# Kernel optimization log

Measured on AMD Instinct MI355X. Metric: run time of the kernel, lower is better.

## Reference

```python
import jax, jax.numpy as jnp
import numpy as np

C_CURV = 1.0
SQRT_C = C_CURV ** 0.5
MAX_NORM = 1.0 / SQRT_C - 1e-5  # project eps == dist clamp eps == 1e-5
EPS = 1e-15


def setup_inputs() -> dict:
    key = jax.random.key(0)
    k1, k2 = jax.random.split(key)
    B, C, D = 4096, 8192, 256
    # points well inside the unit ball: ||x|| ~ 0.05*sqrt(D) ~ 0.8
    x = jax.random.normal(k1, (B, D), dtype=jnp.float32) * 0.05
    # matches nn.Parameter(torch.randn(C, D) * 0.01)
    proto_tangent = jax.random.normal(k2, (C, D), dtype=jnp.float32) * 0.01
    log_scale = jnp.zeros((C,), dtype=jnp.float32)
    return {"x": x, "proto_tangent": proto_tangent, "log_scale": log_scale}


def _expmap0_project(v):
    # exp_0(v) = tanh(sqrt(c)||v||) v / (sqrt(c)||v||), then project onto ball
    vn = jnp.maximum(jnp.linalg.norm(v, axis=-1, keepdims=True), EPS)
    p = jnp.tanh(SQRT_C * vn) * v / (SQRT_C * vn)
    pn = jnp.linalg.norm(p, axis=-1, keepdims=True)
    return jnp.where(pn > MAX_NORM, p / pn * MAX_NORM, p)


def reference(x, proto_tangent, log_scale):
    protos = _expmap0_project(proto_tangent)          # [C, D]
    c = C_CURV
    # mobius_add(-x, y) broadcast over [B, C]; we only need its norm, so use
    # ||a*(-x) + b*y||^2 = a^2||x||^2 - 2ab<x,y> + b^2||y||^2 (same math,
    # avoids materializing the [B, C, D] intermediate the torch code builds).
    x2 = jnp.sum(x * x, axis=-1)[:, None]             # [B, 1]
    y2 = jnp.sum(protos * protos, axis=-1)[None, :]   # [1, C]
    xy = x @ protos.T                                  # [B, C]  <x, y>
    nxy = -xy                                          # <-x, y>
    a = 1.0 + 2.0 * c * nxy + c * y2                   # coeff of (-x)
    b = 1.0 - c * x2                                   # coeff of y
    denom = jnp.maximum(1.0 + 2.0 * c * nxy + (c * c) * x2 * y2, EPS)
    num_sq = a * a * x2 + 2.0 * a * b * nxy + b * b * y2
    norm = jnp.sqrt(jnp.maximum(num_sq, 0.0)) / denom  # ||mobius_add(-x,y)||
    # project clamp (eps=1e-5) and dist clamp (1/sqrt(c)-1e-5) coincide
    norm = jnp.minimum(norm, MAX_NORM)
    dists = (2.0 / SQRT_C) * jnp.arctanh(SQRT_C * norm)  # [B, C]
    return -dists * jnp.exp(log_scale)[None, :]
```

## Files before the change

### kernel.cpp

```cpp
#include <hip/hip_runtime.h>
#include <hip/hip_bf16.h>
#include <cstdint>

#define MAX_NORM (1.0f - 1e-5f)
#define LN2 0.69314718056f
#define WMAX ((1.0f + MAX_NORM) / (1.0f - MAX_NORM))

typedef __attribute__((ext_vector_type(8))) short bf16x8;
typedef __attribute__((ext_vector_type(4))) float f32x4;

__device__ __forceinline__ unsigned short f2bf(float f) {
  union { float f; unsigned int u; } c; c.f = f;
  unsigned int r = c.u + 0x7fffu + ((c.u >> 16) & 1u);
  return (unsigned short)(r >> 16);
}

__device__ __forceinline__ void gld16(const unsigned short* g, unsigned short* l) {
  __builtin_amdgcn_global_load_lds(
      (const __attribute__((address_space(1))) unsigned int*)g,
      (__attribute__((address_space(3))) unsigned int*)l, 16, 0, 0);
}

__global__ void prep_all(const float* __restrict__ x, const float* __restrict__ pt,
                         const float* __restrict__ ls,
                         unsigned short* __restrict__ xbf, unsigned short* __restrict__ pbf,
                         float* __restrict__ x2, float* __restrict__ fx,
                         float* __restrict__ gy, float* __restrict__ hy,
                         float* __restrict__ es2, int M, int N, int D) {
  int row = blockIdx.x * (blockDim.x >> 6) + (threadIdx.x >> 6);
  int lane = threadIdx.x & 63;
  if (row >= M + N) return;
  const bool isX = row < M;
  const int r = isX ? row : row - M;
  const float* src = (isX ? x : pt) + (size_t)r * D;
  f32x4 v = ((const f32x4*)src)[lane];
  float ss = v[0]*v[0] + v[1]*v[1] + v[2]*v[2] + v[3]*v[3];
  #pragma unroll
  for (int off = 32; off >= 1; off >>= 1) ss += __shfl_xor(ss, off);
  float scale = 1.0f;
  float outsq = ss;
  if (!isX) {
    float vn  = sqrtf(ss);
    float vnc = fmaxf(vn, 1e-15f);
    float th  = tanhf(vnc);
    scale = th / vnc;
    float pn = scale * vn;
    if (pn > MAX_NORM) { float pr = MAX_NORM / pn; scale *= pr; pn = MAX_NORM; }
    outsq = pn * pn;
  }
  unsigned short* dst = (isX ? xbf : pbf) + (size_t)r * D + lane * 4;
  unsigned long long pk =
        (unsigned long long)f2bf(v[0]*scale)
      | ((unsigned long long)f2bf(v[1]*scale) << 16)
      | ((unsigned long long)f2bf(v[2]*scale) << 32)
      | ((unsigned long long)f2bf(v[3]*scale) << 48);
  *(unsigned long long*)dst = pk;
  if (lane == 0) {
    if (isX) {
      x2[r] = outsq;
      fx[r] = 2.0f / (1.0f - outsq);
    } else {
      float g = 1.0f / (1.0f - outsq);
      gy[r]  = g;
      hy[r]  = g * outsq;
      es2[r] = -__expf(ls[r]) * LN2;
    }
  }
}

__global__ __launch_bounds__(256, 2)
void hyp_gemm(const unsigned short* __restrict__ xbf,
              const unsigned short* __restrict__ pbf,
              const float* __restrict__ x2, const float* __restrict__ fx,
              const float* __restrict__ gy, const float* __restrict__ hy,
              const float* __restrict__ es2, float* __restrict__ out,
              int M, int N, int K) {
  __shared__ __align__(16) unsigned short As[2][2][128 * 32];
  __shared__ __align__(16) unsigned short Bs[2][2][128 * 32];
  const int t    = threadIdx.x;
  const int wv   = t >> 6;
  const int lane = t & 63;
  const int wr   = wv >> 1, wc = wv & 1;
  const int frow = lane & 15, kgrp = lane >> 4;
  const int nTM  = M >> 7;
  const int tileM = blockIdx.x % nTM;
  const int tileN = blockIdx.x / nTM;
  const int gr0 = tileM * 128 + wr * 64;
  const int gc0 = tileN * 128 + wc * 64;
  const int NT  = K >> 6;

  f32x4 acc[4][4];
  #pragma unroll
  for (int m = 0; m < 4; ++m)
    #pragma unroll
    for (int n = 0; n < 4; ++n) acc[m][n] = (f32x4){0.f, 0.f, 0.f, 0.f};

  const int srow  = wv * 16 + (lane >> 2);
  const int skoff = (lane & 3) * 8;
  const unsigned short* gA = xbf + (size_t)(tileM * 128 + srow) * K + skoff;
  const unsigned short* gB = pbf + (size_t)(tileN * 128 + srow) * K + skoff;
  const size_t rskip = (size_t)64 * K;

#define STAGE(b, kt)                                                           \
  {                                                                            \
    _Pragma("unroll")                                                          \
    for (int p = 0; p < 2; ++p) {                                              \
      _Pragma("unroll")                                                        \
      for (int j = 0; j < 2; ++j) {                                            \
        gld16(gA + (size_t)j * rskip + (kt) * 64 + p * 32,                     \
              &As[b][p][(j * 64 + wv * 16) * 32]);                             \
        gld16(gB + (size_t)j * rskip + (kt) * 64 + p * 32,                     \
              &Bs[b][p][(j * 64 + wv * 16) * 32]);                             \
      }                                                                        \
    }                                                                          \
  }

#define COMPUTE(b)                                                             \
  {                                                                            \
    _Pragma("unroll")                                                          \
    for (int p = 0; p < 2; ++p) {                                              \
      bf16x8 af[4], bg[4];                                                     \
      _Pragma("unroll")                                                        \
      for (int m = 0; m < 4; ++m)                                              \
        af[m] = *(const bf16x8*)&As[b][p][(wr * 64 + m * 16 + frow) * 32 + kgrp * 8]; \
      _Pragma("unroll")                                                        \
      for (int n = 0; n < 4; ++n)                                              \
        bg[n] = *(const bf16x8*)&Bs[b][p][(wc * 64 + n * 16 + frow) * 32 + kgrp * 8]; \
      _Pragma("unroll")                                                        \
      for (int m = 0; m < 4; ++m)                                              \
        _Pragma("unroll")                                                      \
        for (int n = 0; n < 4; ++n)                                            \
          acc[m][n] = __builtin_amdgcn_mfma_f32_16x16x32_bf16(bg[n], af[m], acc[m][n], 0, 0, 0); \
    }                                                                          \
  }

  STAGE(0, 0);
  __syncthreads();
  int cur = 0;
  for (int kt = 0; kt < NT; ++kt) {
    if (kt + 1 < NT) STAGE(cur ^ 1, kt + 1);
    COMPUTE(cur);
    __syncthreads();
    cur ^= 1;
  }
#undef STAGE
#undef COMPUTE

  float x2s[4], fxs[4];
  #pragma unroll
  for (int m = 0; m < 4; ++m) {
    x2s[m] = x2[gr0 + m * 16 + frow];
    fxs[m] = fx[gr0 + m * 16 + frow];
  }
  #pragma unroll
  for (int n = 0; n < 4; ++n) {
    const int c0 = gc0 + n * 16 + kgrp * 4;
    f32x4 gv = *(const f32x4*)(gy  + c0);
    f32x4 hv = *(const f32x4*)(hy  + c0);
    f32x4 ev = *(const f32x4*)(es2 + c0);
    #pragma unroll
    for (int m = 0; m < 4; ++m) {
      f32x4 a4 = acc[m][n];
      f32x4 o;
      #pragma unroll
      for (int r = 0; r < 4; ++r) {
        float xy = a4[r];
        float u  = fmaf(fxs[m], fmaf(gv[r], fmaf(-2.0f, xy, x2s[m]), hv[r]), 1.0f);
        float t2 = fmaxf(fmaf(u, u, -1.0f), 0.0f);
        float w  = u + __builtin_amdgcn_sqrtf(t2);
        w = fminf(w, WMAX);
        o[r] = ev[r] * __log2f(w);
      }
      *(f32x4*)&out[(size_t)(gr0 + m * 16 + frow) * N + c0] = o;
    }
  }
}

extern "C" void kernel_launch(void* const* d_in, const int* in_sizes, int n_in,
                              void* d_out, int out_size, void* d_ws, size_t ws_size,
                              hipStream_t stream) {
  const float* x  = (const float*)d_in[0];
  const float* pt = (const float*)d_in[1];
  const float* ls = (const float*)d_in[2];
  const int Csz = in_sizes[2];
  const int D   = in_sizes[1] / Csz;
  const int Bsz = in_sizes[0] / D;
  const int M = Bsz, N = Csz, K = D;
  float* outp = (float*)d_out;

  char* ws = (char*)d_ws;
  unsigned short* xbf = (unsigned short*)ws; ws += (size_t)M * K * 2;
  unsigned short* pbf = (unsigned short*)ws; ws += (size_t)N * K * 2;
  float* x2  = (float*)ws; ws += (size_t)M * 4;
  float* fx  = (float*)ws; ws += (size_t)M * 4;
  float* gy  = (float*)ws; ws += (size_t)N * 4;
  float* hy  = (float*)ws; ws += (size_t)N * 4;
  float* es2 = (float*)ws; ws += (size_t)N * 4;

  hipLaunchKernelGGL(prep_all, dim3((M + N + 3) / 4), dim3(256), 0, stream,
                     x, pt, ls, xbf, pbf, x2, fx, gy, hy, es2, M, N, K);
  hipLaunchKernelGGL(hyp_gemm, dim3((M / 128) * (N / 128)), dim3(256), 0, stream,
                     xbf, pbf, x2, fx, gy, hy, es2, outp, M, N, K);
}
```

Baseline: 55.58 us.

## Switch GEMM to 32x32x16 MFMA tiles with XOR-swizzled LDS layout

Replaces the 16x16x32 bf16 MFMA tiling (4x4 accumulators per wave) with 32x32x16 MFMA (2x2 f32x16 accumulators). The LDS fill order for the k-chunks is XOR-swizzled so the 32-row fragment reads avoid bank conflicts. The epilogue is remapped to the 32x32 output layout. The aim is fewer LDS fragment loads and a denser MFMA issue. The risk is a different epilogue store pattern and swizzle mistakes that could break correctness.

```diff
diff --git a/kernel.cpp b/kernel.cpp
--- a/kernel.cpp
+++ b/kernel.cpp
@@ -8,6 +8,7 @@
 
 typedef __attribute__((ext_vector_type(8))) short bf16x8;
 typedef __attribute__((ext_vector_type(4))) float f32x4;
+typedef __attribute__((ext_vector_type(16))) float f32x16;
 
 __device__ __forceinline__ unsigned short f2bf(float f) {
   union { float f; unsigned int u; } c; c.f = f;
@@ -81,7 +82,7 @@
   const int wv   = t >> 6;
   const int lane = t & 63;
   const int wr   = wv >> 1, wc = wv & 1;
-  const int frow = lane & 15, kgrp = lane >> 4;
+  const int l31  = lane & 31, hi = lane >> 5;
   const int nTM  = M >> 7;
   const int tileM = blockIdx.x % nTM;
   const int tileN = blockIdx.x / nTM;
@@ -89,17 +90,19 @@
   const int gc0 = tileN * 128 + wc * 64;
   const int NT  = K >> 6;
 
-  f32x4 acc[4][4];
-  #pragma unroll
-  for (int m = 0; m < 4; ++m)
+  f32x16 acc[2][2];
+  #pragma unroll
+  for (int m = 0; m < 2; ++m)
     #pragma unroll
-    for (int n = 0; n < 4; ++n) acc[m][n] = (f32x4){0.f, 0.f, 0.f, 0.f};
+    for (int n = 0; n < 2; ++n) acc[m][n] = (f32x16)(0.0f);
 
   const int srow  = wv * 16 + (lane >> 2);
-  const int skoff = (lane & 3) * 8;
+  const int skoff = ((lane & 3) ^ (((lane >> 3) & 1) << 1)) * 8;
   const unsigned short* gA = xbf + (size_t)(tileM * 128 + srow) * K + skoff;
   const unsigned short* gB = pbf + (size_t)(tileN * 128 + srow) * K + skoff;
   const size_t rskip = (size_t)64 * K;
+
+  const int rswz = ((lane >> 1) & 1) << 1;
 
 #define STAGE(b, kt)                                                           \
   {                                                                            \
@@ -119,18 +122,23 @@
   {                                                                            \
     _Pragma("unroll")                                                          \
     for (int p = 0; p < 2; ++p) {                                              \
-      bf16x8 af[4], bg[4];                                                     \
+      bf16x8 af[2][2], bg[2][2];                                               \
       _Pragma("unroll")                                                        \
-      for (int m = 0; m < 4; ++m)                                              \
-        af[m] = *(const bf16x8*)&As[b][p][(wr * 64 + m * 16 + frow) * 32 + kgrp * 8]; \
+      for (int m = 0; m < 2; ++m)                                              \
+        _Pragma("unroll")                                                      \
+        for (int ks = 0; ks < 2; ++ks) {                                       \
+          const int kqa = (ks * 2 + hi) ^ rswz;                                \
+          af[m][ks] = *(const bf16x8*)&As[b][p][(wr * 64 + m * 32 + l31) * 32 + kqa * 8]; \
+          bg[m][ks] = *(const bf16x8*)&Bs[b][p][(wc * 64 + m * 32 + l31) * 32 + kqa * 8]; \
+        }                                                                      \
       _Pragma("unroll")                                                        \
-      for (int n = 0; n < 4; ++n)                                              \
-        bg[n] = *(const bf16x8*)&Bs[b][p][(wc * 64 + n * 16 + frow) * 32 + kgrp * 8]; \
-      _Pragma("unroll")                                                        \
-      for (int m = 0; m < 4; ++m)                                              \
+      for (int m = 0; m < 2; ++m)                                              \
         _Pragma("unroll")                                                      \
-        for (int n = 0; n < 4; ++n)                                            \
-          acc[m][n] = __builtin_amdgcn_mfma_f32_16x16x32_bf16(bg[n], af[m], acc[m][n], 0, 0, 0); \
+        for (int n = 0; n < 2; ++n)                                            \
+          _Pragma("unroll")                                                    \
+          for (int ks = 0; ks < 2; ++ks)                                       \
+            acc[m][n] = __builtin_amdgcn_mfma_f32_32x32x16_bf16(               \
+                bg[n][ks], af[m][ks], acc[m][n], 0, 0, 0);                     \
     }                                                                          \
   }
 
@@ -146,32 +154,34 @@
 #undef STAGE
 #undef COMPUTE
 
-  float x2s[4], fxs[4];
-  #pragma unroll
-  for (int m = 0; m < 4; ++m) {
-    x2s[m] = x2[gr0 + m * 16 + frow];
-    fxs[m] = fx[gr0 + m * 16 + frow];
-  }
-  #pragma unroll
-  for (int n = 0; n < 4; ++n) {
-    const int c0 = gc0 + n * 16 + kgrp * 4;
-    f32x4 gv = *(const f32x4*)(gy  + c0);
-    f32x4 hv = *(const f32x4*)(hy  + c0);
-    f32x4 ev = *(const f32x4*)(es2 + c0);
+  float x2s[2], fxs[2];
+  #pragma unroll
+  for (int m = 0; m < 2; ++m) {
+    x2s[m] = x2[gr0 + m * 32 + l31];
+    fxs[m] = fx[gr0 + m * 32 + l31];
+  }
+  #pragma unroll
+  for (int n = 0; n < 2; ++n) {
     #pragma unroll
-    for (int m = 0; m < 4; ++m) {
-      f32x4 a4 = acc[m][n];
-      f32x4 o;
+    for (int g = 0; g < 4; ++g) {
+      const int c0 = gc0 + n * 32 + g * 8 + hi * 4;
+      f32x4 gv = *(const f32x4*)(gy  + c0);
+      f32x4 hv = *(const f32x4*)(hy  + c0);
+      f32x4 ev = *(const f32x4*)(es2 + c0);
       #pragma unroll
-      for (int r = 0; r < 4; ++r) {
-        float xy = a4[r];
-        float u  = fmaf(fxs[m], fmaf(gv[r], fmaf(-2.0f, xy, x2s[m]), hv[r]), 1.0f);
-        float t2 = fmaxf(fmaf(u, u, -1.0f), 0.0f);
-        float w  = u + __builtin_amdgcn_sqrtf(t2);
-        w = fminf(w, WMAX);
-        o[r] = ev[r] * __log2f(w);
+      for (int m = 0; m < 2; ++m) {
+        f32x4 o;
+        #pragma unroll
+        for (int r = 0; r < 4; ++r) {
+          float xy = acc[m][n][g * 4 + r];
+          float u  = fmaf(fxs[m], fmaf(gv[r], fmaf(-2.0f, xy, x2s[m]), hv[r]), 1.0f);
+          float t2 = fmaxf(fmaf(u, u, -1.0f), 0.0f);
+          float w  = u + __builtin_amdgcn_sqrtf(t2);
+          w = fminf(w, WMAX);
+          o[r] = ev[r] * __log2f(w);
+        }
+        *(f32x4*)&out[(size_t)(gr0 + m * 32 + l31) * N + c0] = o;
       }
-      *(f32x4*)&out[(size_t)(gr0 + m * 16 + frow) * N + c0] = o;
     }
   }
 }
```

New measurement: 62.44 us. 1.12x slower.

## Load MFMA operands directly from global memory, dropping LDS staging

Applied to the files above, without the earlier changes.

Removes the double-buffered LDS staging through global_load_lds and the per-iteration barriers. Each wave now loads its bf16 A/B fragments straight from global memory into registers, in a fully unrolled loop over K=256. Occupancy is raised to 3 blocks per SM. Global traffic per block roughly doubles because the two waves sharing a tile row or column no longer share data, so the kernel leans on L2/L1 caching. K is also hardcoded to 256.

```diff
diff --git a/kernel.cpp b/kernel.cpp
--- a/kernel.cpp
+++ b/kernel.cpp
@@ -13,12 +13,6 @@
   union { float f; unsigned int u; } c; c.f = f;
   unsigned int r = c.u + 0x7fffu + ((c.u >> 16) & 1u);
   return (unsigned short)(r >> 16);
-}
-
-__device__ __forceinline__ void gld16(const unsigned short* g, unsigned short* l) {
-  __builtin_amdgcn_global_load_lds(
-      (const __attribute__((address_space(1))) unsigned int*)g,
-      (__attribute__((address_space(3))) unsigned int*)l, 16, 0, 0);
 }
 
 __global__ void prep_all(const float* __restrict__ x, const float* __restrict__ pt,
@@ -68,15 +62,13 @@
   }
 }
 
-__global__ __launch_bounds__(256, 2)
+__global__ __launch_bounds__(256, 3)
 void hyp_gemm(const unsigned short* __restrict__ xbf,
               const unsigned short* __restrict__ pbf,
               const float* __restrict__ x2, const float* __restrict__ fx,
               const float* __restrict__ gy, const float* __restrict__ hy,
               const float* __restrict__ es2, float* __restrict__ out,
               int M, int N, int K) {
-  __shared__ __align__(16) unsigned short As[2][2][128 * 32];
-  __shared__ __align__(16) unsigned short Bs[2][2][128 * 32];
   const int t    = threadIdx.x;
   const int wv   = t >> 6;
   const int lane = t & 63;
@@ -87,7 +79,6 @@
   const int tileN = blockIdx.x / nTM;
   const int gr0 = tileM * 128 + wr * 64;
   const int gc0 = tileN * 128 + wc * 64;
-  const int NT  = K >> 6;
 
   f32x4 acc[4][4];
   #pragma unroll
@@ -95,56 +86,28 @@
     #pragma unroll
     for (int n = 0; n < 4; ++n) acc[m][n] = (f32x4){0.f, 0.f, 0.f, 0.f};
 
-  const int srow  = wv * 16 + (lane >> 2);
-  const int skoff = (lane & 3) * 8;
-  const unsigned short* gA = xbf + (size_t)(tileM * 128 + srow) * K + skoff;
-  const unsigned short* gB = pbf + (size_t)(tileN * 128 + srow) * K + skoff;
-  const size_t rskip = (size_t)64 * K;
+  const unsigned short* pA[4];
+  const unsigned short* pB[4];
+  #pragma unroll
+  for (int m = 0; m < 4; ++m)
+    pA[m] = xbf + (size_t)(gr0 + m * 16 + frow) * K + kgrp * 8;
+  #pragma unroll
+  for (int n = 0; n < 4; ++n)
+    pB[n] = pbf + (size_t)(gc0 + n * 16 + frow) * K + kgrp * 8;
 
-#define STAGE(b, kt)                                                           \
-  {                                                                            \
-    _Pragma("unroll")                                                          \
-    for (int p = 0; p < 2; ++p) {                                              \
-      _Pragma("unroll")                                                        \
-      for (int j = 0; j < 2; ++j) {                                            \
-        gld16(gA + (size_t)j * rskip + (kt) * 64 + p * 32,                     \
-              &As[b][p][(j * 64 + wv * 16) * 32]);                             \
-        gld16(gB + (size_t)j * rskip + (kt) * 64 + p * 32,                     \
-              &Bs[b][p][(j * 64 + wv * 16) * 32]);                             \
-      }                                                                        \
-    }                                                                          \
+  #pragma unroll
+  for (int k0 = 0; k0 < 256; k0 += 32) {
+    bf16x8 af[4], bg[4];
+    #pragma unroll
+    for (int m = 0; m < 4; ++m) af[m] = *(const bf16x8*)(pA[m] + k0);
+    #pragma unroll
+    for (int n = 0; n < 4; ++n) bg[n] = *(const bf16x8*)(pB[n] + k0);
+    #pragma unroll
+    for (int m = 0; m < 4; ++m)
+      #pragma unroll
+      for (int n = 0; n < 4; ++n)
+        acc[m][n] = __builtin_amdgcn_mfma_f32_16x16x32_bf16(bg[n], af[m], acc[m][n], 0, 0, 0);
   }
-
-#define COMPUTE(b)                                                             \
-  {                                                                            \
-    _Pragma("unroll")                                                          \
-    for (int p = 0; p < 2; ++p) {                                              \
-      bf16x8 af[4], bg[4];                                                     \
-      _Pragma("unroll")                                                        \
-      for (int m = 0; m < 4; ++m)                                              \
-        af[m] = *(const bf16x8*)&As[b][p][(wr * 64 + m * 16 + frow) * 32 + kgrp * 8]; \
-      _Pragma("unroll")                                                        \
-      for (int n = 0; n < 4; ++n)                                              \
-        bg[n] = *(const bf16x8*)&Bs[b][p][(wc * 64 + n * 16 + frow) * 32 + kgrp * 8]; \
-      _Pragma("unroll")                                                        \
-      for (int m = 0; m < 4; ++m)                                              \
-        _Pragma("unroll")                                                      \
-        for (int n = 0; n < 4; ++n)                                            \
-          acc[m][n] = __builtin_amdgcn_mfma_f32_16x16x32_bf16(bg[n], af[m], acc[m][n], 0, 0, 0); \
-    }                                                                          \
-  }
-
-  STAGE(0, 0);
-  __syncthreads();
-  int cur = 0;
-  for (int kt = 0; kt < NT; ++kt) {
-    if (kt + 1 < NT) STAGE(cur ^ 1, kt + 1);
-    COMPUTE(cur);
-    __syncthreads();
-    cur ^= 1;
-  }
-#undef STAGE
-#undef COMPUTE
 
   float x2s[4], fxs[4];
   #pragma unroll
```

New measurement: 84.00 us. +51.1%, slower.

## Process four N-tiles per block, overlapping previous tile's epilogue with next tile's MFMA

Applied to the files above, without the earlier changes.

Each block now computes four consecutive 128-column output tiles, using two accumulator sets so that the transcendental epilogue and stores of the previous tile are interleaved, one slice at a time, with the K-loop MFMAs of the current tile. The K loop is fully unrolled to four steps, which assumes K equals 256, and the next tile's first stage is prefetched during the last step. This aims to hide the epilogue's compute and store time and to amortise block startup. In exchange it doubles accumulator register use, which risks spills or lower occupancy, and it cuts the grid size by a factor of four.

```diff
diff --git a/kernel.cpp b/kernel.cpp
--- a/kernel.cpp
+++ b/kernel.cpp
@@ -83,68 +83,18 @@
   const int wr   = wv >> 1, wc = wv & 1;
   const int frow = lane & 15, kgrp = lane >> 4;
   const int nTM  = M >> 7;
-  const int tileM = blockIdx.x % nTM;
-  const int tileN = blockIdx.x / nTM;
+  const int tileM  = blockIdx.x % nTM;
+  const int tileN0 = (blockIdx.x / nTM) * 4;
   const int gr0 = tileM * 128 + wr * 64;
-  const int gc0 = tileN * 128 + wc * 64;
-  const int NT  = K >> 6;
-
-  f32x4 acc[4][4];
-  #pragma unroll
-  for (int m = 0; m < 4; ++m)
-    #pragma unroll
-    for (int n = 0; n < 4; ++n) acc[m][n] = (f32x4){0.f, 0.f, 0.f, 0.f};
+
+  f32x4 accA[4][4], accB[4][4];
 
   const int srow  = wv * 16 + (lane >> 2);
   const int skoff = (lane & 3) * 8;
-  const unsigned short* gA = xbf + (size_t)(tileM * 128 + srow) * K + skoff;
-  const unsigned short* gB = pbf + (size_t)(tileN * 128 + srow) * K + skoff;
+  const unsigned short* gA  = xbf + (size_t)(tileM * 128 + srow) * K + skoff;
+  const unsigned short* gB0 = pbf + (size_t)(tileN0 * 128 + srow) * K + skoff;
   const size_t rskip = (size_t)64 * K;
-
-#define STAGE(b, kt)                                                           \
-  {                                                                            \
-    _Pragma("unroll")                                                          \
-    for (int p = 0; p < 2; ++p) {                                              \
-      _Pragma("unroll")                                                        \
-      for (int j = 0; j < 2; ++j) {                                            \
-        gld16(gA + (size_t)j * rskip + (kt) * 64 + p * 32,                     \
-              &As[b][p][(j * 64 + wv * 16) * 32]);                             \
-        gld16(gB + (size_t)j * rskip + (kt) * 64 + p * 32,                     \
-              &Bs[b][p][(j * 64 + wv * 16) * 32]);                             \
-      }                                                                        \
-    }                                                                          \
-  }
-
-#define COMPUTE(b)                                                             \
-  {                                                                            \
-    _Pragma("unroll")                                                          \
-    for (int p = 0; p < 2; ++p) {                                              \
-      bf16x8 af[4], bg[4];                                                     \
-      _Pragma("unroll")                                                        \
-      for (int m = 0; m < 4; ++m)                                              \
-        af[m] = *(const bf16x8*)&As[b][p][(wr * 64 + m * 16 + frow) * 32 + kgrp * 8]; \
-      _Pragma("unroll")                                                        \
-      for (int n = 0; n < 4; ++n)                                              \
-        bg[n] = *(const bf16x8*)&Bs[b][p][(wc * 64 + n * 16 + frow) * 32 + kgrp * 8]; \
-      _Pragma("unroll")                                                        \
-      for (int m = 0; m < 4; ++m)                                              \
-        _Pragma("unroll")                                                      \
-        for (int n = 0; n < 4; ++n)                                            \
-          acc[m][n] = __builtin_amdgcn_mfma_f32_16x16x32_bf16(bg[n], af[m], acc[m][n], 0, 0, 0); \
-    }                                                                          \
-  }
-
-  STAGE(0, 0);
-  __syncthreads();
-  int cur = 0;
-  for (int kt = 0; kt < NT; ++kt) {
-    if (kt + 1 < NT) STAGE(cur ^ 1, kt + 1);
-    COMPUTE(cur);
-    __syncthreads();
-    cur ^= 1;
-  }
-#undef STAGE
-#undef COMPUTE
+  const size_t nskip = (size_t)128 * K;
 
   float x2s[4], fxs[4];
   #pragma unroll
@@ -152,28 +102,93 @@
     x2s[m] = x2[gr0 + m * 16 + frow];
     fxs[m] = fx[gr0 + m * 16 + frow];
   }
+
+#define STAGE(b, kt, GBP)                                                      \
+  {                                                                            \
+    _Pragma("unroll")                                                          \
+    for (int p = 0; p < 2; ++p) {                                              \
+      _Pragma("unroll")                                                        \
+      for (int j = 0; j < 2; ++j) {                                            \
+        gld16(gA + (size_t)j * rskip + (kt) * 64 + p * 32,                     \
+              &As[b][p][(j * 64 + wv * 16) * 32]);                             \
+        gld16((GBP) + (size_t)j * rskip + (kt) * 64 + p * 32,                  \
+              &Bs[b][p][(j * 64 + wv * 16) * 32]);                             \
+      }                                                                        \
+    }                                                                          \
+  }
+
+#define COMPUTE(b, ACC)                                                        \
+  {                                                                            \
+    _Pragma("unroll")                                                          \
+    for (int p = 0; p < 2; ++p) {                                              \
+      bf16x8 af[4], bg[4];                                                     \
+      _Pragma("unroll")                                                        \
+      for (int m = 0; m < 4; ++m)                                              \
+        af[m] = *(const bf16x8*)&As[b][p][(wr * 64 + m * 16 + frow) * 32 + kgrp * 8]; \
+      _Pragma("unroll")                                                        \
+      for (int n = 0; n < 4; ++n)                                              \
+        bg[n] = *(const bf16x8*)&Bs[b][p][(wc * 64 + n * 16 + frow) * 32 + kgrp * 8]; \
+      _Pragma("unroll")                                                        \
+      for (int m = 0; m < 4; ++m)                                              \
+        _Pragma("unroll")                                                      \
+        for (int n = 0; n < 4; ++n)                                            \
+          ACC[m][n] = __builtin_amdgcn_mfma_f32_16x16x32_bf16(bg[n], af[m], ACC[m][n], 0, 0, 0); \
+    }                                                                          \
+  }
+
+#define EPI_SLICE(ACC, TNP, NN)                                                \
+  {                                                                            \
+    const int c0 = (tileN0 + (TNP)) * 128 + wc * 64 + (NN) * 16 + kgrp * 4;    \
+    f32x4 gv = *(const f32x4*)(gy  + c0);                                      \
+    f32x4 hv = *(const f32x4*)(hy  + c0);                                      \
+    f32x4 ev = *(const f32x4*)(es2 + c0);                                      \
+    _Pragma("unroll")                                                          \
+    for (int m = 0; m < 4; ++m) {                                              \
+      f32x4 a4 = ACC[m][(NN)];                                                 \
+      f32x4 o;                                                                 \
+      _Pragma("unroll")                                                        \
+      for (int r = 0; r < 4; ++r) {                                            \
+        float xy = a4[r];                                                      \
+        float u  = fmaf(fxs[m], fmaf(gv[r], fmaf(-2.0f, xy, x2s[m]), hv[r]), 1.0f); \
+        float t2 = fmaxf(fmaf(u, u, -1.0f), 0.0f);                             \
+        float w  = fminf(u + __builtin_amdgcn_sqrtf(t2), WMAX);                \
+        o[r] = ev[r] * __log2f(w);                                             \
+      }                                                                        \
+      *(f32x4*)&out[(size_t)(gr0 + m * 16 + frow) * N + c0] = o;               \
+    }                                                                          \
+  }
+
+#define TILE(TN, ACCC, ACCP)                                                   \
+  {                                                                            \
+    _Pragma("unroll")                                                          \
+    for (int m = 0; m < 4; ++m)                                                \
+      _Pragma("unroll")                                                        \
+      for (int n = 0; n < 4; ++n) ACCC[m][n] = (f32x4){0.f, 0.f, 0.f, 0.f};    \
+    __syncthreads();                                                           \
+    _Pragma("unroll")                                                          \
+    for (int kt = 0; kt < 4; ++kt) {                                           \
+      if (kt < 3)          STAGE(cur ^ 1, kt + 1, gB0 + (TN) * nskip)          \
+      else if ((TN) < 3)   STAGE(cur ^ 1, 0, gB0 + ((TN) + 1) * nskip)         \
+      if ((TN) > 0)        EPI_SLICE(ACCP, (TN) - 1, kt)                       \
+      COMPUTE(cur, ACCC)                                                       \
+      __syncthreads();                                                         \
+      cur ^= 1;                                                                \
+    }                                                                          \
+  }
+
+  STAGE(0, 0, gB0)
+  int cur = 0;
+  TILE(0, accA, accB)
+  TILE(1, accB, accA)
+  TILE(2, accA, accB)
+  TILE(3, accB, accA)
   #pragma unroll
-  for (int n = 0; n < 4; ++n) {
-    const int c0 = gc0 + n * 16 + kgrp * 4;
-    f32x4 gv = *(const f32x4*)(gy  + c0);
-    f32x4 hv = *(const f32x4*)(hy  + c0);
-    f32x4 ev = *(const f32x4*)(es2 + c0);
-    #pragma unroll
-    for (int m = 0; m < 4; ++m) {
-      f32x4 a4 = acc[m][n];
-      f32x4 o;
-      #pragma unroll
-      for (int r = 0; r < 4; ++r) {
-        float xy = a4[r];
-        float u  = fmaf(fxs[m], fmaf(gv[r], fmaf(-2.0f, xy, x2s[m]), hv[r]), 1.0f);
-        float t2 = fmaxf(fmaf(u, u, -1.0f), 0.0f);
-        float w  = u + __builtin_amdgcn_sqrtf(t2);
-        w = fminf(w, WMAX);
-        o[r] = ev[r] * __log2f(w);
-      }
-      *(f32x4*)&out[(size_t)(gr0 + m * 16 + frow) * N + c0] = o;
-    }
-  }
+  for (int n = 0; n < 4; ++n) EPI_SLICE(accB, 3, n)
+
+#undef TILE
+#undef EPI_SLICE
+#undef COMPUTE
+#undef STAGE
 }
 
 extern "C" void kernel_launch(void* const* d_in, const int* in_sizes, int n_in,
@@ -199,6 +214,6 @@
 
   hipLaunchKernelGGL(prep_all, dim3((M + N + 3) / 4), dim3(256), 0, stream,
                      x, pt, ls, xbf, pbf, x2, fx, gy, hy, es2, M, N, K);
-  hipLaunchKernelGGL(hyp_gemm, dim3((M / 128) * (N / 128)), dim3(256), 0, stream,
+  hipLaunchKernelGGL(hyp_gemm, dim3((M / 128) * (N / 512)), dim3(256), 0, stream,
                      xbf, pbf, x2, fx, gy, hy, es2, outp, M, N, K);
 }
```

Result: faster. 53.15 us (-4.4%).
